# Performance work log

Hardware: AMD Instinct MI355X
Metric: run time of the kernel (lower is better)

## Reference

```python
import math
import jax, jax.numpy as jnp
import numpy as np

INVALID_VALUE = -0.1  # ChannelPositions.INVALID_VALUE sentinel
POS_DIM = 288
MARGIN = 0.2
N_FREQS = 12  # int(sqrt(POS_DIM // 2))


def fourier_emb(positions):
    # positions: [..., 2] in [0, 1]; returns [..., POS_DIM]
    freqs = jnp.arange(N_FREQS, dtype=positions.dtype)
    width = 1.0 + 2.0 * MARGIN
    pos = positions + MARGIN
    p = (2.0 * math.pi / width) * freqs  # [K]
    # loc[..., i, j] = pos_x * p[i] + pos_y * p[j]
    loc = pos[..., None, None, 0] * p[:, None] + pos[..., None, None, 1] * p[None, :]
    loc = loc.reshape(*positions.shape[:-1], N_FREQS * N_FREQS)  # [..., 144]
    return jnp.concatenate([jnp.cos(loc), jnp.sin(loc)], axis=-1)  # [..., 288]


def setup_inputs() -> dict:
    key = jax.random.key(0)
    k1, k2, k3, k4 = jax.random.split(key, 4)
    B, C, T = 128, 273, 2048
    chout, n_subjects = 270, 200
    meg = jax.random.normal(k1, (B, C, T), dtype=jnp.float32)
    positions = jax.random.uniform(k2, (B, C, 2), dtype=jnp.float32)
    subject_ids = jax.random.randint(k3, (B,), 0, n_subjects)
    heads = jax.random.normal(k4, (n_subjects, chout, POS_DIM), dtype=jnp.float32) / math.sqrt(POS_DIM)
    return {"meg": meg, "positions": positions, "subject_ids": subject_ids, "heads": heads}


def reference(meg, positions, subject_ids, heads):
    # meg: [B,C,T], positions: [B,C,2], subject_ids: [B], heads: [S,O,D]
    emb = fourier_emb(positions)            # [B,C,D]
    h = heads[subject_ids]                  # per-subject gather -> [B,O,D]
    scores = jnp.einsum('bcd,bod->boc', emb, h)  # [B,O,C]
    invalid = jnp.all(positions == INVALID_VALUE, axis=-1)  # [B,C]
    scores = jnp.where(invalid[:, None, :], -jnp.inf, scores)
    weights = jax.nn.softmax(scores, axis=2)     # over channels C
    out = jnp.einsum('bct,boc->bot', meg, weights)  # [B,O,T]
    return out
```

## Files before the change

kernel.cpp:

```cpp
#include <hip/hip_runtime.h>
#include <math.h>

#define B_ 128
#define C_ 273
#define T_ 2048
#define O_ 270
#define D_ 288
#define OP_ 288
#define CP_ 384
#define KP_ 288

typedef __attribute__((ext_vector_type(8))) short short8;
typedef __attribute__((ext_vector_type(4))) float f32x4;

__device__ inline ushort f2bf(float f) {
    uint u = __float_as_uint(f);
    return (ushort)((u + 0x7FFFu + ((u >> 16) & 1u)) >> 16);
}
__device__ inline uint pack2bf(float lo, float hi) {
    return (uint)f2bf(lo) | ((uint)f2bf(hi) << 16);
}

__global__ __launch_bounds__(256) void k_emb(const float* __restrict__ pos,
                                             ushort* __restrict__ emb) {
    int idx = blockIdx.x * 256 + threadIdx.x;
    const int total = B_ * CP_ * 144;
    if (idx >= total) return;
    int bc = idx / 144;
    int k  = idx - bc * 144;
    int b  = bc / CP_;
    int c  = bc - b * CP_;
    ushort* row = emb + ((size_t)b * CP_ + c) * D_;
    if (c >= C_) { row[k] = 0; row[144 + k] = 0; return; }
    int i = k / 12, j = k - i * 12;
    float px = pos[((size_t)b * C_ + c) * 2 + 0] + 0.2f;
    float py = pos[((size_t)b * C_ + c) * 2 + 1] + 0.2f;
    const float w0 = 4.48798950512827605f;
    float loc = px * (w0 * (float)i) + py * (w0 * (float)j);
    float s, cc;
    sincosf(loc, &s, &cc);
    row[k]       = f2bf(cc);
    row[144 + k] = f2bf(s);
}

__global__ __launch_bounds__(256) void k_gather(const float* __restrict__ heads,
                                                const int* __restrict__ sids,
                                                ushort* __restrict__ hb) {
    int idx = blockIdx.x * 256 + threadIdx.x;
    const int total = B_ * OP_ * (D_ / 8);
    if (idx >= total) return;
    int d8 = (idx % 36) * 8;
    int t  = idx / 36;
    int o  = t % OP_;
    int b  = t / OP_;
    uint4 outv = make_uint4(0, 0, 0, 0);
    if (o < O_) {
        int sid = sids[b];
        const float* src = heads + ((size_t)sid * O_ + o) * D_ + d8;
        float4 v0 = *(const float4*)src;
        float4 v1 = *(const float4*)(src + 4);
        outv.x = pack2bf(v0.x, v0.y); outv.y = pack2bf(v0.z, v0.w);
        outv.z = pack2bf(v1.x, v1.y); outv.w = pack2bf(v1.z, v1.w);
    }
    *(uint4*)(hb + ((size_t)b * OP_ + o) * D_ + d8) = outv;
}

__global__ __launch_bounds__(256) void k_scores(const ushort* __restrict__ hb,
                                                const ushort* __restrict__ emb,
                                                float* __restrict__ scores) {
    __shared__ uint AsU[96 * 16];
    __shared__ uint BsU[128 * 16];
    int b  = blockIdx.z;
    int o0 = blockIdx.y * 96;
    int n0 = blockIdx.x * 128;
    int tid = threadIdx.x;
    int wid = tid >> 6, lane = tid & 63;
    int wm = wid >> 1, wn = wid & 1;
    int lm = lane & 15, lq = lane >> 4;
    const ushort* Ab = hb  + (size_t)b * OP_ * D_;
    const ushort* Bb = emb + (size_t)b * CP_ * D_;
    f32x4 acc[3][4];
    #pragma unroll
    for (int i = 0; i < 3; ++i)
        #pragma unroll
        for (int j = 0; j < 4; ++j) { f32x4 z = {0.f, 0.f, 0.f, 0.f}; acc[i][j] = z; }

    for (int k0 = 0; k0 < D_; k0 += 32) {
        {
            int row = tid >> 2, ch = tid & 3;
            uint4 v = *(const uint4*)(Ab + (size_t)(o0 + row) * D_ + k0 + ch * 8);
            *(uint4*)&AsU[tid * 4] = v;
            if (tid < 128) {
                int s2 = 256 + tid, row2 = s2 >> 2, ch2 = s2 & 3;
                uint4 v2 = *(const uint4*)(Ab + (size_t)(o0 + row2) * D_ + k0 + ch2 * 8);
                *(uint4*)&AsU[s2 * 4] = v2;
            }
        }
        #pragma unroll
        for (int it = 0; it < 2; ++it) {
            int slot = tid + it * 256;
            int row = slot >> 2, ch = slot & 3;
            uint4 v = *(const uint4*)(Bb + (size_t)(n0 + row) * D_ + k0 + ch * 8);
            *(uint4*)&BsU[slot * 4] = v;
        }
        __syncthreads();
        short8 a[3], bb[4];
        #pragma unroll
        for (int fm = 0; fm < 3; ++fm)
            a[fm] = *(short8*)((ushort*)AsU + (wm * 48 + fm * 16 + lm) * 32 + lq * 8);
        #pragma unroll
        for (int fn = 0; fn < 4; ++fn)
            bb[fn] = *(short8*)((ushort*)BsU + (wn * 64 + fn * 16 + lm) * 32 + lq * 8);
        #pragma unroll
        for (int fm = 0; fm < 3; ++fm)
            #pragma unroll
            for (int fn = 0; fn < 4; ++fn)
                acc[fm][fn] = __builtin_amdgcn_mfma_f32_16x16x32_bf16(a[fm], bb[fn], acc[fm][fn], 0, 0, 0);
        __syncthreads();
    }
    #pragma unroll
    for (int fm = 0; fm < 3; ++fm) {
        int obase = o0 + wm * 48 + fm * 16 + lq * 4;
        #pragma unroll
        for (int fn = 0; fn < 4; ++fn) {
            int c = n0 + wn * 64 + fn * 16 + lm;
            if (c >= C_) continue;
            #pragma unroll
            for (int r = 0; r < 4; ++r) {
                int o = obase + r;
                if (o < O_) scores[((size_t)b * O_ + o) * C_ + c] = acc[fm][fn][r];
            }
        }
    }
}

__global__ __launch_bounds__(256) void k_softmax(const float* __restrict__ scores,
                                                 const float* __restrict__ pos,
                                                 ushort* __restrict__ wbf) {
    int wave = threadIdx.x >> 6, lane = threadIdx.x & 63;
    int row = blockIdx.x * 4 + wave;
    if (row >= B_ * OP_) return;
    int b = row / OP_, o = row - b * OP_;
    ushort* wrow = wbf + ((size_t)b * OP_ + o) * KP_;
    if (o >= O_) {
        #pragma unroll
        for (int ch = 0; ch < 5; ++ch) { int c = lane + ch * 64; if (c < KP_) wrow[c] = 0; }
        return;
    }
    const float* srow = scores + ((size_t)b * O_ + o) * C_;
    const float* prow = pos + (size_t)b * C_ * 2;
    float v[5];
    float m = -INFINITY;
    #pragma unroll
    for (int ch = 0; ch < 5; ++ch) {
        int c = lane + ch * 64;
        float s = -INFINITY;
        if (c < C_) {
            s = srow[c];
            float px = prow[c * 2], py = prow[c * 2 + 1];
            if (px == -0.1f && py == -0.1f) s = -INFINITY;
        }
        v[ch] = s;
        m = fmaxf(m, s);
    }
    #pragma unroll
    for (int off = 32; off; off >>= 1) m = fmaxf(m, __shfl_xor(m, off, 64));
    float sum = 0.f;
    #pragma unroll
    for (int ch = 0; ch < 5; ++ch) {
        v[ch] = expf(v[ch] - m);
        if (lane + ch * 64 < C_) sum += v[ch];
    }
    #pragma unroll
    for (int off = 32; off; off >>= 1) sum += __shfl_xor(sum, off, 64);
    float inv = 1.0f / sum;
    #pragma unroll
    for (int ch = 0; ch < 5; ++ch) {
        int c = lane + ch * 64;
        if (c < C_) wrow[c] = f2bf(v[ch] * inv);
        else if (c < KP_) wrow[c] = 0;
    }
}

__global__ __launch_bounds__(256) void k_out(const float* __restrict__ meg,
                                             const ushort* __restrict__ wbf,
                                             float* __restrict__ out) {
    __shared__ uint AsU[96 * 16];
    __shared__ uint BsU[128 * 16];
    int b  = blockIdx.z;
    int o0 = blockIdx.y * 96;
    int t0 = blockIdx.x * 128;
    int tid = threadIdx.x;
    int wid = tid >> 6, lane = tid & 63;
    int wm = wid >> 1, wn = wid & 1;
    int lm = lane & 15, lq = lane >> 4;
    const ushort* Ab = wbf + (size_t)b * OP_ * KP_;
    const float*  Mb = meg + (size_t)b * C_ * T_;
    f32x4 acc[3][4];
    #pragma unroll
    for (int i = 0; i < 3; ++i)
        #pragma unroll
        for (int j = 0; j < 4; ++j) { f32x4 z = {0.f, 0.f, 0.f, 0.f}; acc[i][j] = z; }

    int cpair = tid & 15;
    int tq0   = tid >> 4;

    for (int k0 = 0; k0 < KP_; k0 += 32) {
        {
            int row = tid >> 2, ch = tid & 3;
            uint4 v = *(const uint4*)(Ab + (size_t)(o0 + row) * KP_ + k0 + ch * 8);
            *(uint4*)&AsU[tid * 4] = v;
            if (tid < 128) {
                int s2 = 256 + tid, row2 = s2 >> 2, ch2 = s2 & 3;
                uint4 v2 = *(const uint4*)(Ab + (size_t)(o0 + row2) * KP_ + k0 + ch2 * 8);
                *(uint4*)&AsU[s2 * 4] = v2;
            }
        }
        #pragma unroll
        for (int it = 0; it < 2; ++it) {
            int tqq = tq0 + it * 16;
            int c   = k0 + cpair * 2;
            int t   = tqq * 4;
            float4 v0 = make_float4(0.f, 0.f, 0.f, 0.f);
            float4 v1 = make_float4(0.f, 0.f, 0.f, 0.f);
            if (c < C_)     v0 = *(const float4*)(Mb + (size_t)c * T_ + t0 + t);
            if (c + 1 < C_) v1 = *(const float4*)(Mb + (size_t)(c + 1) * T_ + t0 + t);
            BsU[(t + 0) * 16 + cpair] = pack2bf(v0.x, v1.x);
            BsU[(t + 1) * 16 + cpair] = pack2bf(v0.y, v1.y);
            BsU[(t + 2) * 16 + cpair] = pack2bf(v0.z, v1.z);
            BsU[(t + 3) * 16 + cpair] = pack2bf(v0.w, v1.w);
        }
        __syncthreads();
        short8 a[3], bb[4];
        #pragma unroll
        for (int fm = 0; fm < 3; ++fm)
            a[fm] = *(short8*)((ushort*)AsU + (wm * 48 + fm * 16 + lm) * 32 + lq * 8);
        #pragma unroll
        for (int fn = 0; fn < 4; ++fn)
            bb[fn] = *(short8*)((ushort*)BsU + (wn * 64 + fn * 16 + lm) * 32 + lq * 8);
        #pragma unroll
        for (int fm = 0; fm < 3; ++fm)
            #pragma unroll
            for (int fn = 0; fn < 4; ++fn)
                acc[fm][fn] = __builtin_amdgcn_mfma_f32_16x16x32_bf16(a[fm], bb[fn], acc[fm][fn], 0, 0, 0);
        __syncthreads();
    }
    #pragma unroll
    for (int fm = 0; fm < 3; ++fm) {
        int obase = o0 + wm * 48 + fm * 16 + lq * 4;
        #pragma unroll
        for (int fn = 0; fn < 4; ++fn) {
            int t = t0 + wn * 64 + fn * 16 + lm;
            #pragma unroll
            for (int r = 0; r < 4; ++r) {
                int o = obase + r;
                if (o < O_) out[((size_t)b * O_ + o) * T_ + t] = acc[fm][fn][r];
            }
        }
    }
}

extern "C" void kernel_launch(void* const* d_in, const int* in_sizes, int n_in,
                              void* d_out, int out_size, void* d_ws, size_t ws_size,
                              hipStream_t stream) {
    const float* meg   = (const float*)d_in[0];
    const float* pos   = (const float*)d_in[1];
    const int*   sids  = (const int*)d_in[2];
    const float* heads = (const float*)d_in[3];
    float* out = (float*)d_out;

    ushort* emb = (ushort*)d_ws;
    ushort* wbf = (ushort*)d_ws;
    ushort* hb  = emb + (size_t)B_ * CP_ * D_;
    float* scores = (float*)(hb + (size_t)B_ * OP_ * D_);

    k_emb<<<(B_ * CP_ * 144 + 255) / 256, 256, 0, stream>>>(pos, emb);
    k_gather<<<(B_ * OP_ * 36 + 255) / 256, 256, 0, stream>>>(heads, sids, hb);
    k_scores<<<dim3(3, 3, B_), 256, 0, stream>>>(hb, emb, scores);
    k_softmax<<<(B_ * OP_ + 3) / 4, 256, 0, stream>>>(scores, pos, wbf);
    k_out<<<dim3(T_ / 128, 3, B_), 256, 0, stream>>>(meg, wbf, out);
}
```

Measured before the change: 668.6 us.

## Pre-transpose meg to bf16 and double-buffer both GEMMs with direct global-to-LDS loads

Adds a kernel that transposes meg into a bf16 [B,T,C] layout with padded channels. The output GEMM then streams both operands through double-buffered LDS using global_load_lds, instead of converting fp32 meg inside the GEMM. The scores GEMM gets the same double-buffered direct-to-LDS staging. The sincos and exp calls are swapped for the fast intrinsics. This costs an extra pass over meg plus the megT write and read, and it only runs when the workspace is large enough; otherwise the old fused kernel is kept.

Measured after the change: 708.6 us. 1.06x slower.

```diff
diff --git a/kernel.cpp b/kernel.cpp
--- a/kernel.cpp
+++ b/kernel.cpp
@@ -38,7 +38,7 @@
     const float w0 = 4.48798950512827605f;
     float loc = px * (w0 * (float)i) + py * (w0 * (float)j);
     float s, cc;
-    sincosf(loc, &s, &cc);
+    __sincosf(loc, &s, &cc);
     row[k]       = f2bf(cc);
     row[144 + k] = f2bf(s);
 }
@@ -65,11 +65,25 @@
     *(uint4*)(hb + ((size_t)b * OP_ + o) * D_ + d8) = outv;
 }
 
+__device__ inline void stage_ab(const ushort* __restrict__ A0,
+                                const ushort* __restrict__ B0,
+                                uint* buf, int wid, int lane) {
+    for (int ch = wid; ch < 14; ch += 4) {
+        bool isA = ch < 6;
+        int slotb = (isA ? ch : ch - 6) << 6;
+        int slot  = slotb + lane;
+        const ushort* g = (isA ? A0 : B0) + (size_t)(slot >> 2) * KP_ + ((slot & 3) << 3);
+        uint* dst = buf + (isA ? (slotb << 2) : (1536 + (slotb << 2)));
+        __builtin_amdgcn_global_load_lds(
+            (const __attribute__((address_space(1))) uint*)g,
+            (__attribute__((address_space(3))) uint*)dst, 16, 0, 0);
+    }
+}
+
 __global__ __launch_bounds__(256) void k_scores(const ushort* __restrict__ hb,
                                                 const ushort* __restrict__ emb,
                                                 float* __restrict__ scores) {
-    __shared__ uint AsU[96 * 16];
-    __shared__ uint BsU[128 * 16];
+    __shared__ uint LdsU[2 * 3584];
     int b  = blockIdx.z;
     int o0 = blockIdx.y * 96;
     int n0 = blockIdx.x * 128;
@@ -77,47 +91,43 @@
     int wid = tid >> 6, lane = tid & 63;
     int wm = wid >> 1, wn = wid & 1;
     int lm = lane & 15, lq = lane >> 4;
-    const ushort* Ab = hb  + (size_t)b * OP_ * D_;
-    const ushort* Bb = emb + (size_t)b * CP_ * D_;
+    const ushort* Ab = hb  + ((size_t)b * OP_ + o0) * D_;
+    const ushort* Bb = emb + ((size_t)b * CP_ + n0) * D_;
     f32x4 acc[3][4];
     #pragma unroll
     for (int i = 0; i < 3; ++i)
         #pragma unroll
         for (int j = 0; j < 4; ++j) { f32x4 z = {0.f, 0.f, 0.f, 0.f}; acc[i][j] = z; }
 
-    for (int k0 = 0; k0 < D_; k0 += 32) {
-        {
-            int row = tid >> 2, ch = tid & 3;
-            uint4 v = *(const uint4*)(Ab + (size_t)(o0 + row) * D_ + k0 + ch * 8);
-            *(uint4*)&AsU[tid * 4] = v;
-            if (tid < 128) {
-                int s2 = 256 + tid, row2 = s2 >> 2, ch2 = s2 & 3;
-                uint4 v2 = *(const uint4*)(Ab + (size_t)(o0 + row2) * D_ + k0 + ch2 * 8);
-                *(uint4*)&AsU[s2 * 4] = v2;
-            }
-        }
-        #pragma unroll
-        for (int it = 0; it < 2; ++it) {
-            int slot = tid + it * 256;
-            int row = slot >> 2, ch = slot & 3;
-            uint4 v = *(const uint4*)(Bb + (size_t)(n0 + row) * D_ + k0 + ch * 8);
-            *(uint4*)&BsU[slot * 4] = v;
-        }
+    auto compute = [&](int cb) {
+        const ushort* As = (const ushort*)(LdsU + cb * 3584);
+        const ushort* Bs = (const ushort*)(LdsU + cb * 3584 + 1536);
+        short8 a[3], bv[4];
+        #pragma unroll
+        for (int fm = 0; fm < 3; ++fm)
+            a[fm] = *(const short8*)(As + (wm * 48 + fm * 16 + lm) * 32 + lq * 8);
+        #pragma unroll
+        for (int fn = 0; fn < 4; ++fn)
+            bv[fn] = *(const short8*)(Bs + (wn * 64 + fn * 16 + lm) * 32 + lq * 8);
+        #pragma unroll
+        for (int fm = 0; fm < 3; ++fm)
+            #pragma unroll
+            for (int fn = 0; fn < 4; ++fn)
+                acc[fm][fn] = __builtin_amdgcn_mfma_f32_16x16x32_bf16(a[fm], bv[fn], acc[fm][fn], 0, 0, 0);
+    };
+
+    int cur = 0;
+    stage_ab(Ab, Bb, LdsU, wid, lane);
+    __syncthreads();
+    for (int k = 0; k < 8; ++k) {
+        int nk = (k + 1) * 32;
+        stage_ab(Ab + nk, Bb + nk, LdsU + (cur ^ 1) * 3584, wid, lane);
+        compute(cur);
         __syncthreads();
-        short8 a[3], bb[4];
-        #pragma unroll
-        for (int fm = 0; fm < 3; ++fm)
-            a[fm] = *(short8*)((ushort*)AsU + (wm * 48 + fm * 16 + lm) * 32 + lq * 8);
-        #pragma unroll
-        for (int fn = 0; fn < 4; ++fn)
-            bb[fn] = *(short8*)((ushort*)BsU + (wn * 64 + fn * 16 + lm) * 32 + lq * 8);
-        #pragma unroll
-        for (int fm = 0; fm < 3; ++fm)
-            #pragma unroll
-            for (int fn = 0; fn < 4; ++fn)
-                acc[fm][fn] = __builtin_amdgcn_mfma_f32_16x16x32_bf16(a[fm], bb[fn], acc[fm][fn], 0, 0, 0);
-        __syncthreads();
-    }
+        cur ^= 1;
+    }
+    compute(cur);
+
     #pragma unroll
     for (int fm = 0; fm < 3; ++fm) {
         int obase = o0 + wm * 48 + fm * 16 + lq * 4;
@@ -168,7 +178,7 @@
     float sum = 0.f;
     #pragma unroll
     for (int ch = 0; ch < 5; ++ch) {
-        v[ch] = expf(v[ch] - m);
+        v[ch] = __expf(v[ch] - m);
         if (lane + ch * 64 < C_) sum += v[ch];
     }
     #pragma unroll
@@ -182,9 +192,108 @@
     }
 }
 
-__global__ __launch_bounds__(256) void k_out(const float* __restrict__ meg,
+__global__ __launch_bounds__(256) void k_megT(const float* __restrict__ meg,
+                                              ushort* __restrict__ megT) {
+    __shared__ float lds[64 * 65];
+    int b  = blockIdx.z;
+    int t0 = blockIdx.x * 64;
+    int c0 = blockIdx.y * 64;
+    int tid = threadIdx.x;
+    const float* Mb = meg + (size_t)b * C_ * T_;
+    #pragma unroll
+    for (int i = 0; i < 4; ++i) {
+        int slot = tid + i * 256;
+        int r = slot >> 4, q = slot & 15;
+        float4 v = make_float4(0.f, 0.f, 0.f, 0.f);
+        if (c0 + r < C_) v = *(const float4*)(Mb + (size_t)(c0 + r) * T_ + t0 + q * 4);
+        lds[r * 65 + q * 4 + 0] = v.x;
+        lds[r * 65 + q * 4 + 1] = v.y;
+        lds[r * 65 + q * 4 + 2] = v.z;
+        lds[r * 65 + q * 4 + 3] = v.w;
+    }
+    __syncthreads();
+    ushort* Tb = megT + (size_t)b * T_ * KP_;
+    #pragma unroll
+    for (int i = 0; i < 2; ++i) {
+        int slot = tid + i * 256;
+        int t = slot >> 3, co = (slot & 7) * 8;
+        int c = c0 + co;
+        if (c >= KP_) continue;
+        uint4 w;
+        w.x = pack2bf(lds[(co + 0) * 65 + t], lds[(co + 1) * 65 + t]);
+        w.y = pack2bf(lds[(co + 2) * 65 + t], lds[(co + 3) * 65 + t]);
+        w.z = pack2bf(lds[(co + 4) * 65 + t], lds[(co + 5) * 65 + t]);
+        w.w = pack2bf(lds[(co + 6) * 65 + t], lds[(co + 7) * 65 + t]);
+        *(uint4*)(Tb + (size_t)(t0 + t) * KP_ + c) = w;
+    }
+}
+
+__global__ __launch_bounds__(256) void k_out(const ushort* __restrict__ megT,
                                              const ushort* __restrict__ wbf,
                                              float* __restrict__ out) {
+    __shared__ uint LdsU[2 * 3584];
+    int b  = blockIdx.z;
+    int o0 = blockIdx.y * 96;
+    int t0 = blockIdx.x * 128;
+    int tid = threadIdx.x;
+    int wid = tid >> 6, lane = tid & 63;
+    int wm = wid >> 1, wn = wid & 1;
+    int lm = lane & 15, lq = lane >> 4;
+    const ushort* Ab = wbf  + ((size_t)b * OP_ + o0) * KP_;
+    const ushort* Bb = megT + ((size_t)b * T_ + t0) * KP_;
+    f32x4 acc[3][4];
+    #pragma unroll
+    for (int i = 0; i < 3; ++i)
+        #pragma unroll
+        for (int j = 0; j < 4; ++j) { f32x4 z = {0.f, 0.f, 0.f, 0.f}; acc[i][j] = z; }
+
+    auto compute = [&](int cb) {
+        const ushort* As = (const ushort*)(LdsU + cb * 3584);
+        const ushort* Bs = (const ushort*)(LdsU + cb * 3584 + 1536);
+        short8 a[3], bv[4];
+        #pragma unroll
+        for (int fm = 0; fm < 3; ++fm)
+            a[fm] = *(const short8*)(As + (wm * 48 + fm * 16 + lm) * 32 + lq * 8);
+        #pragma unroll
+        for (int fn = 0; fn < 4; ++fn)
+            bv[fn] = *(const short8*)(Bs + (wn * 64 + fn * 16 + lm) * 32 + lq * 8);
+        #pragma unroll
+        for (int fm = 0; fm < 3; ++fm)
+            #pragma unroll
+            for (int fn = 0; fn < 4; ++fn)
+                acc[fm][fn] = __builtin_amdgcn_mfma_f32_16x16x32_bf16(a[fm], bv[fn], acc[fm][fn], 0, 0, 0);
+    };
+
+    int cur = 0;
+    stage_ab(Ab, Bb, LdsU, wid, lane);
+    __syncthreads();
+    for (int k = 0; k < 8; ++k) {
+        int nk = (k + 1) * 32;
+        stage_ab(Ab + nk, Bb + nk, LdsU + (cur ^ 1) * 3584, wid, lane);
+        compute(cur);
+        __syncthreads();
+        cur ^= 1;
+    }
+    compute(cur);
+
+    #pragma unroll
+    for (int fm = 0; fm < 3; ++fm) {
+        int obase = o0 + wm * 48 + fm * 16 + lq * 4;
+        #pragma unroll
+        for (int fn = 0; fn < 4; ++fn) {
+            int t = t0 + wn * 64 + fn * 16 + lm;
+            #pragma unroll
+            for (int r = 0; r < 4; ++r) {
+                int o = obase + r;
+                if (o < O_) out[((size_t)b * O_ + o) * T_ + t] = acc[fm][fn][r];
+            }
+        }
+    }
+}
+
+__global__ __launch_bounds__(256) void k_out_fused(const float* __restrict__ meg,
+                                                   const ushort* __restrict__ wbf,
+                                                   float* __restrict__ out) {
     __shared__ uint AsU[96 * 16];
     __shared__ uint BsU[128 * 16];
     int b  = blockIdx.z;
@@ -269,14 +378,23 @@
     const float* heads = (const float*)d_in[3];
     float* out = (float*)d_out;
 
+    const size_t embElems = (size_t)B_ * CP_ * D_;
+    const size_t hbElems  = (size_t)B_ * OP_ * D_;
     ushort* emb = (ushort*)d_ws;
-    ushort* wbf = (ushort*)d_ws;
-    ushort* hb  = emb + (size_t)B_ * CP_ * D_;
-    float* scores = (float*)(hb + (size_t)B_ * OP_ * D_);
+    ushort* wbf = emb;
+    ushort* hb  = emb + embElems;
+    float* scores = (float*)(hb + hbElems);
+    ushort* megT  = hb;
+    const size_t need_new = embElems * 2 + (size_t)B_ * T_ * KP_ * 2;
 
     k_emb<<<(B_ * CP_ * 144 + 255) / 256, 256, 0, stream>>>(pos, emb);
     k_gather<<<(B_ * OP_ * 36 + 255) / 256, 256, 0, stream>>>(heads, sids, hb);
     k_scores<<<dim3(3, 3, B_), 256, 0, stream>>>(hb, emb, scores);
     k_softmax<<<(B_ * OP_ + 3) / 4, 256, 0, stream>>>(scores, pos, wbf);
-    k_out<<<dim3(T_ / 128, 3, B_), 256, 0, stream>>>(meg, wbf, out);
-}
+    if (ws_size >= need_new) {
+        k_megT<<<dim3(T_ / 64, 5, B_), 256, 0, stream>>>(meg, megT);
+        k_out<<<dim3(T_ / 128, 3, B_), 256, 0, stream>>>(megT, wbf, out);
+    } else {
+        k_out_fused<<<dim3(T_ / 128, 3, B_), 256, 0, stream>>>(meg, wbf, out);
+    }
+}
```
